# Kernel optimization log

Hardware: AMD Instinct MI355X
Metric: run time of the kernel (lower is better)

The kernel has to match this reference:

```python
import jax, jax.numpy as jnp
import numpy as np

N, E, IN, HID, OUT, H = 10000, 320000, 256, 128, 128, 4
SLOPE = 0.2

def setup_inputs() -> dict:
    key = jax.random.key(0)
    ks = jax.random.split(key, 12)
    s = lambda d: 1.0 / np.sqrt(d)
    return {
        "x": jax.random.normal(ks[0], (N, IN), jnp.float32),
        "edge_index": jax.random.randint(ks[1], (2, E), 0, N, jnp.int32),
        "W1": jax.random.normal(ks[2], (IN, H * HID), jnp.float32) * s(IN),
        "a_src1": jax.random.normal(ks[3], (H, HID), jnp.float32) * s(HID),
        "a_dst1": jax.random.normal(ks[4], (H, HID), jnp.float32) * s(HID),
        "b1": jnp.zeros((H * HID,), jnp.float32),
        "W2": jax.random.normal(ks[5], (H * HID, H * OUT), jnp.float32) * s(H * HID),
        "a_src2": jax.random.normal(ks[6], (H, OUT), jnp.float32) * s(OUT),
        "a_dst2": jax.random.normal(ks[7], (H, OUT), jnp.float32) * s(OUT),
        "b2": jnp.zeros((OUT,), jnp.float32),
    }

def _gat_layer(x, src, dst, W, a_src, a_dst, bias, concat, C):
    n = x.shape[0]
    h = (x @ W).reshape(n, H, C)                      # [N,H,C]
    alpha_s = jnp.einsum('nhc,hc->nh', h, a_src)      # [N,H]
    alpha_d = jnp.einsum('nhc,hc->nh', h, a_dst)
    e = jax.nn.leaky_relu(alpha_s[src] + alpha_d[dst], SLOPE)  # [E,H]
    # segment softmax over incoming edges of each dst node
    m = jax.ops.segment_max(e, dst, num_segments=n)   # [N,H]
    m = jnp.where(jnp.isfinite(m), m, 0.0)
    ex = jnp.exp(e - m[dst])
    denom = jax.ops.segment_sum(ex, dst, num_segments=n)
    alpha = ex / (denom[dst] + 1e-16)                 # [E,H]
    msg = h[src] * alpha[:, :, None]                  # [E,H,C]
    out = jax.ops.segment_sum(msg, dst, num_segments=n)  # [N,H,C]
    out = out.reshape(n, H * C) if concat else out.mean(axis=1)
    return out + bias

def reference(x, edge_index, W1, a_src1, a_dst1, b1, W2, a_src2, a_dst2, b2):
    n = x.shape[0]
    loops = jnp.arange(n, dtype=edge_index.dtype)
    src = jnp.concatenate([edge_index[0], loops])
    dst = jnp.concatenate([edge_index[1], loops])
    h = _gat_layer(x, src, dst, W1, a_src1, a_dst1, b1, True, HID)
    h = jax.nn.relu(h)  # dropout is identity in eval mode
    out = _gat_layer(h, src, dst, W2, a_src2, a_dst2, b2, False, OUT)
    return out
```

## Files before the change

kernel.cpp:

```cpp
#include <hip/hip_runtime.h>
#include <hip/hip_fp16.h>
#include <math.h>

#define Nn 10000
#define Ee 320000
#define EE 330000
#define INF_ 256
#define NH 4
#define OUTC 128
#define F1 512
#define F2 512
#define SLOPE 0.2f
#define STRIDE 80
#define LDK 40
#define NT 256
#define GRID 1024
#define GT (GRID * NT)
#define MT 157
#define GEMM_TILES (MT * NH)
#define PASS_VB ((Nn / 16) * NH)

static __device__ __forceinline__ float lrelu(float x) { return fmaxf(x, SLOPE * x); }

using frag_ab = __attribute__((ext_vector_type(8))) _Float16;
using frag_c  = __attribute__((ext_vector_type(4))) float;

struct Params {
    const float* x; const int* ei;
    const float* W1; const float* a_src1; const float* a_dst1; const float* b1;
    const float* W2; const float* a_src2; const float* a_dst2; const float* b2;
    float* out;
    int* counts; int* csr; int* bar;
    _Float16* hh; _Float16* aggh; _Float16* w1t; _Float16* w2t; _Float16* tmp;
    float* as1; float* ad1; float* as2; float* ad2;
};

static __device__ __forceinline__ void gbar(int* bar, int ph) {
    __syncthreads();
    if (threadIdx.x == 0) {
        __hip_atomic_fetch_add(&bar[ph], 1, __ATOMIC_ACQ_REL, __HIP_MEMORY_SCOPE_AGENT);
        while (__hip_atomic_load(&bar[ph], __ATOMIC_ACQUIRE, __HIP_MEMORY_SCOPE_AGENT) < GRID)
            __builtin_amdgcn_s_sleep(1);
    }
    __syncthreads();
}

static __device__ void prep0(const Params& p) {
    int gt = blockIdx.x * NT + threadIdx.x;
    for (int i = gt; i < Nn; i += GT) p.counts[i] = 0;
    for (int i = gt; i < F1 * INF_; i += GT) {
        int n = i >> 8, k = i & 255;
        p.w1t[i] = (_Float16)p.W1[(size_t)k * F1 + n];
    }
    for (int i = gt; i < F2 * F1; i += GT) {
        int n = i >> 9, k = i & 511;
        p.w2t[i] = (_Float16)p.W2[(size_t)k * F2 + n];
    }
}

static __device__ void scatter_edges(const Params& p, int bi, int nb) {
    for (int e = bi * NT + threadIdx.x; e < EE; e += nb * NT) {
        int src, dst;
        if (e < Ee) { src = p.ei[e]; dst = p.ei[Ee + e]; }
        else        { src = e - Ee; dst = e - Ee; }
        int slot = atomicAdd(&p.counts[dst], 1);
        if (slot < STRIDE) p.csr[dst * STRIDE + slot] = src;
    }
}

template <bool AF32>
static __device__ void gemm_tile(const _Float16* __restrict__ Ah,
                                 const float* __restrict__ Af,
                                 const _Float16* __restrict__ BT,
                                 _Float16* __restrict__ C,
                                 const float* __restrict__ a_src,
                                 const float* __restrict__ a_dst,
                                 float* __restrict__ as_out,
                                 float* __restrict__ ad_out,
                                 int K, int bmi, int head,
                                 _Float16* As, _Float16* Bs) {
    const int tid = threadIdx.x;
    const int wave = tid >> 6, lane = tid & 63;
    const int q = lane >> 4, ml = lane & 15;
    const int bm = bmi * 64, bn = head * 128;
    const int srow = tid >> 2, scol = (tid & 3) * 8;

    frag_c acc[8];
#pragma unroll
    for (int f = 0; f < 8; f++)
#pragma unroll
        for (int r = 0; r < 4; r++) acc[f][r] = 0.f;

    for (int k0 = 0; k0 < K; k0 += 32) {
        int gm = bm + srow;
        frag_ab av;
        if (gm < Nn) {
            if constexpr (AF32) {
                const float* Ap = Af + (size_t)gm * K + k0 + scol;
                float4 v0 = *(const float4*)Ap;
                float4 v1 = *(const float4*)(Ap + 4);
                av[0] = (_Float16)v0.x; av[1] = (_Float16)v0.y;
                av[2] = (_Float16)v0.z; av[3] = (_Float16)v0.w;
                av[4] = (_Float16)v1.x; av[5] = (_Float16)v1.y;
                av[6] = (_Float16)v1.z; av[7] = (_Float16)v1.w;
            } else {
                av = *(const frag_ab*)(Ah + (size_t)gm * K + k0 + scol);
            }
        } else {
#pragma unroll
            for (int j = 0; j < 8; j++) av[j] = (_Float16)0.f;
        }
        *(frag_ab*)&As[srow * LDK + scol] = av;
        *(frag_ab*)&Bs[srow * LDK + scol] =
            *(const frag_ab*)(BT + (size_t)(bn + srow) * K + k0 + scol);
        *(frag_ab*)&Bs[(64 + srow) * LDK + scol] =
            *(const frag_ab*)(BT + (size_t)(bn + 64 + srow) * K + k0 + scol);
        __syncthreads();
        frag_ab a = *(frag_ab*)&As[(wave * 16 + ml) * LDK + q * 8];
#pragma unroll
        for (int f = 0; f < 8; f++) {
            frag_ab b = *(frag_ab*)&Bs[(f * 16 + ml) * LDK + q * 8];
            acc[f] = __builtin_amdgcn_mfma_f32_16x16x32_f16(a, b, acc[f], 0, 0, 0);
        }
        __syncthreads();
    }
    float asum[4] = {}, dsum[4] = {};
#pragma unroll
    for (int f = 0; f < 8; f++) {
        int cl = f * 16 + ml;
        int col = bn + cl;
        float sa = a_src[head * 128 + cl];
        float da = a_dst[head * 128 + cl];
#pragma unroll
        for (int r = 0; r < 4; r++) {
            int row = bm + wave * 16 + q * 4 + r;
            if (row < Nn) C[(size_t)row * (NH * 128) + col] = (_Float16)acc[f][r];
            asum[r] += acc[f][r] * sa;
            dsum[r] += acc[f][r] * da;
        }
    }
#pragma unroll
    for (int r = 0; r < 4; r++) {
#pragma unroll
        for (int off = 1; off < 16; off <<= 1) {
            asum[r] += __shfl_xor(asum[r], off);
            dsum[r] += __shfl_xor(dsum[r], off);
        }
    }
    if (ml == 0) {
#pragma unroll
        for (int r = 0; r < 4; r++) {
            int row = bm + wave * 16 + q * 4 + r;
            if (row < Nn) {
                as_out[(size_t)head * Nn + row] = asum[r];
                ad_out[(size_t)head * Nn + row] = dsum[r];
            }
        }
    }
}

template <int LAYER>
static __device__ void pass_body(int vb, const int* __restrict__ counts,
                                 const int* __restrict__ csr,
                                 const float* __restrict__ as,
                                 const float* __restrict__ ad,
                                 const _Float16* __restrict__ hh,
                                 const float* __restrict__ b1,
                                 _Float16* __restrict__ outp, int2 (*ew)[84]) {
    int head = vb & 3;
    int qw = threadIdx.x >> 4;
    int l = threadIdx.x & 15;
    int n = (vb >> 2) * 16 + qw;
    int deg = counts[n]; if (deg > STRIDE) deg = STRIDE;
    int pdeg = (deg + 7) & ~7;
    const float* ash = as + (size_t)head * Nn;
    float adh = ad[(size_t)head * Nn + n];
    int base = n * STRIDE;
    float m = -1e30f;
    for (int k = l; k < pdeg; k += 16) {
        int src = 0; float v = -1e30f;
        if (k < deg) {
            src = csr[base + k];
            v = lrelu(ash[src] + adh);
        }
        ew[qw][k] = make_int2(src, __float_as_int(v));
        m = fmaxf(m, v);
    }
    m = fmaxf(m, __shfl_xor(m, 1));
    m = fmaxf(m, __shfl_xor(m, 2));
    m = fmaxf(m, __shfl_xor(m, 4));
    m = fmaxf(m, __shfl_xor(m, 8));
    float s = 0.f;
    for (int k = l; k < pdeg; k += 16) {
        float e = __expf(__int_as_float(ew[qw][k].y) - m);
        ew[qw][k].y = __float_as_int(e);
        s += e;
    }
    s += __shfl_xor(s, 1);
    s += __shfl_xor(s, 2);
    s += __shfl_xor(s, 4);
    s += __shfl_xor(s, 8);
    float inv = 1.f / (s + 1e-16f);
    int c = head * 128 + (l << 3);
    float acc[8] = {};
    for (int kk = 0; kk < pdeg; kk += 8) {
        int2 pj[8];
#pragma unroll
        for (int j = 0; j < 8; j++) pj[j] = ew[qw][kk + j];
#pragma unroll
        for (int j = 0; j < 8; j++) {
            float w = __int_as_float(pj[j].y);
            frag_ab r = *(const frag_ab*)(hh + (size_t)pj[j].x * 512 + c);
#pragma unroll
            for (int u = 0; u < 8; u++) acc[u] = fmaf((float)r[u], w, acc[u]);
        }
    }
    _Float16 oh[8];
    if constexpr (LAYER == 1) {
#pragma unroll
        for (int j = 0; j < 8; j++)
            oh[j] = (_Float16)fmaxf(acc[j] * inv + b1[c + j], 0.f);
    } else {
        float qq = 0.25f * inv;
#pragma unroll
        for (int j = 0; j < 8; j++) oh[j] = (_Float16)(acc[j] * qq);
    }
    *(float4*)&outp[(size_t)n * 512 + c] = *(float4*)oh;
}

static __device__ void reduce_out(const Params& p) {
    int gt = blockIdx.x * NT + threadIdx.x;
    for (int i = gt; i < Nn * OUTC; i += GT) {
        int n = i >> 7, oc = i & 127;
        const _Float16* tp = p.tmp + (size_t)n * 512 + oc;
        p.out[i] = (float)tp[0] + (float)tp[128] + (float)tp[256] + (float)tp[384] + p.b2[oc];
    }
}

__global__ __launch_bounds__(NT, 4) void mega(Params p) {
    __shared__ _Float16 As[64 * LDK];
    __shared__ _Float16 Bs[128 * LDK];
    __shared__ int2 ew[16][84];

    prep0(p);
    gbar(p.bar, 0);

    if (blockIdx.x < GEMM_TILES)
        gemm_tile<true>(nullptr, p.x, p.w1t, p.hh, p.a_src1, p.a_dst1, p.as1, p.ad1,
                        INF_, blockIdx.x % MT, blockIdx.x / MT, As, Bs);
    else
        scatter_edges(p, blockIdx.x - GEMM_TILES, GRID - GEMM_TILES);
    gbar(p.bar, 1);

    for (int vb = blockIdx.x; vb < PASS_VB; vb += GRID)
        pass_body<1>(vb, p.counts, p.csr, p.as1, p.ad1, p.hh, p.b1, p.aggh, ew);
    gbar(p.bar, 2);

    if (blockIdx.x < GEMM_TILES)
        gemm_tile<false>(p.aggh, nullptr, p.w2t, p.hh, p.a_src2, p.a_dst2, p.as2, p.ad2,
                         F1, blockIdx.x % MT, blockIdx.x / MT, As, Bs);
    gbar(p.bar, 3);

    for (int vb = blockIdx.x; vb < PASS_VB; vb += GRID)
        pass_body<2>(vb, p.counts, p.csr, p.as2, p.ad2, p.hh, nullptr, p.tmp, ew);
    gbar(p.bar, 4);

    reduce_out(p);
}

__global__ __launch_bounds__(NT) void k_p0(Params p) { prep0(p); }
__global__ __launch_bounds__(NT) void k_p1(Params p) {
    __shared__ _Float16 As[64 * LDK];
    __shared__ _Float16 Bs[128 * LDK];
    if (blockIdx.x < GEMM_TILES)
        gemm_tile<true>(nullptr, p.x, p.w1t, p.hh, p.a_src1, p.a_dst1, p.as1, p.ad1,
                        INF_, blockIdx.x % MT, blockIdx.x / MT, As, Bs);
    else
        scatter_edges(p, blockIdx.x - GEMM_TILES, GRID - GEMM_TILES);
}
__global__ __launch_bounds__(NT) void k_p2(Params p) {
    __shared__ int2 ew[16][84];
    for (int vb = blockIdx.x; vb < PASS_VB; vb += GRID)
        pass_body<1>(vb, p.counts, p.csr, p.as1, p.ad1, p.hh, p.b1, p.aggh, ew);
}
__global__ __launch_bounds__(NT) void k_p3(Params p) {
    __shared__ _Float16 As[64 * LDK];
    __shared__ _Float16 Bs[128 * LDK];
    if (blockIdx.x < GEMM_TILES)
        gemm_tile<false>(p.aggh, nullptr, p.w2t, p.hh, p.a_src2, p.a_dst2, p.as2, p.ad2,
                         F1, blockIdx.x % MT, blockIdx.x / MT, As, Bs);
}
__global__ __launch_bounds__(NT) void k_p4(Params p) {
    __shared__ int2 ew[16][84];
    for (int vb = blockIdx.x; vb < PASS_VB; vb += GRID)
        pass_body<2>(vb, p.counts, p.csr, p.as2, p.ad2, p.hh, nullptr, p.tmp, ew);
}
__global__ __launch_bounds__(NT) void k_p5(Params p) { reduce_out(p); }

extern "C" void kernel_launch(void* const* d_in, const int* in_sizes, int n_in,
                              void* d_out, int out_size, void* d_ws, size_t ws_size,
                              hipStream_t stream) {
    Params p;
    p.x      = (const float*)d_in[0];
    p.ei     = (const int*)d_in[1];
    p.W1     = (const float*)d_in[2];
    p.a_src1 = (const float*)d_in[3];
    p.a_dst1 = (const float*)d_in[4];
    p.b1     = (const float*)d_in[5];
    p.W2     = (const float*)d_in[6];
    p.a_src2 = (const float*)d_in[7];
    p.a_dst2 = (const float*)d_in[8];
    p.b2     = (const float*)d_in[9];
    p.out    = (float*)d_out;

    char* w = (char*)d_ws;
    p.tmp  = (_Float16*)w; w += (size_t)Nn * F2 * 2;
    p.hh   = (_Float16*)w; w += (size_t)Nn * F1 * 2;
    p.aggh = (_Float16*)w; w += (size_t)Nn * F1 * 2;
    p.w1t  = (_Float16*)w; w += (size_t)F1 * INF_ * 2;
    p.w2t  = (_Float16*)w; w += (size_t)F2 * F1 * 2;
    p.as1  = (float*)w;    w += (size_t)NH * Nn * 4;
    p.ad1  = (float*)w;    w += (size_t)NH * Nn * 4;
    p.as2  = (float*)w;    w += (size_t)NH * Nn * 4;
    p.ad2  = (float*)w;    w += (size_t)NH * Nn * 4;
    p.csr  = (int*)w;      w += (size_t)Nn * STRIDE * 4;
    p.counts = (int*)w;    w += (size_t)Nn * 4;
    p.bar  = (int*)w;      w += 8 * 4;

    static int occ = -1;
    if (occ < 0) {
        int nb = 0;
        if (hipOccupancyMaxActiveBlocksPerMultiprocessor(&nb, mega, NT, 0) != hipSuccess)
            nb = 0;
        occ = nb;
    }

    if (occ >= 4) {
        (void)hipMemsetAsync(p.bar, 0, 8 * sizeof(int), stream);
        mega<<<GRID, NT, 0, stream>>>(p);
    } else {
        k_p0<<<GRID, NT, 0, stream>>>(p);
        k_p1<<<GRID, NT, 0, stream>>>(p);
        k_p2<<<GRID, NT, 0, stream>>>(p);
        k_p3<<<GEMM_TILES, NT, 0, stream>>>(p);
        k_p4<<<GRID, NT, 0, stream>>>(p);
        k_p5<<<GRID, NT, 0, stream>>>(p);
    }
}
```

Baseline: 198.0 us.

## Size persistent grid from occupancy and alias shared memory between phases

The persistent megakernel now takes its grid size from the occupancy query (occ*256, capped at 1024) instead of a fixed 1024 blocks. The grid barrier reads gridDim, and the GEMM and edge-scatter work loops over tiles so any grid size covers the work. GEMM tiles and the edge-weight buffer now share one aliased shared-memory array, and the launch_bounds minimum-blocks hint is dropped, which may change register allocation and occupancy. The GEMM K-loop moves its trailing barrier to the top of the iteration. This makes the megakernel path usable when fewer than four blocks fit per CU, at the cost of fewer blocks doing more work each when occupancy is lower.

```diff
diff --git a/kernel.cpp b/kernel.cpp
--- a/kernel.cpp
+++ b/kernel.cpp
@@ -14,11 +14,11 @@
 #define STRIDE 80
 #define LDK 40
 #define NT 256
-#define GRID 1024
-#define GT (GRID * NT)
+#define GRID_MAX 1024
 #define MT 157
 #define GEMM_TILES (MT * NH)
 #define PASS_VB ((Nn / 16) * NH)
+#define SMEM_BYTES (192 * LDK * 2)
 
 static __device__ __forceinline__ float lrelu(float x) { return fmaxf(x, SLOPE * x); }
 
@@ -39,20 +39,21 @@
     __syncthreads();
     if (threadIdx.x == 0) {
         __hip_atomic_fetch_add(&bar[ph], 1, __ATOMIC_ACQ_REL, __HIP_MEMORY_SCOPE_AGENT);
-        while (__hip_atomic_load(&bar[ph], __ATOMIC_ACQUIRE, __HIP_MEMORY_SCOPE_AGENT) < GRID)
+        while (__hip_atomic_load(&bar[ph], __ATOMIC_ACQUIRE, __HIP_MEMORY_SCOPE_AGENT) <
+               (int)gridDim.x)
             __builtin_amdgcn_s_sleep(1);
     }
     __syncthreads();
 }
 
-static __device__ void prep0(const Params& p) {
+static __device__ void prep0(const Params& p, int gstride) {
     int gt = blockIdx.x * NT + threadIdx.x;
-    for (int i = gt; i < Nn; i += GT) p.counts[i] = 0;
-    for (int i = gt; i < F1 * INF_; i += GT) {
+    for (int i = gt; i < Nn; i += gstride) p.counts[i] = 0;
+    for (int i = gt; i < F1 * INF_; i += gstride) {
         int n = i >> 8, k = i & 255;
         p.w1t[i] = (_Float16)p.W1[(size_t)k * F1 + n];
     }
-    for (int i = gt; i < F2 * F1; i += GT) {
+    for (int i = gt; i < F2 * F1; i += gstride) {
         int n = i >> 9, k = i & 511;
         p.w2t[i] = (_Float16)p.W2[(size_t)k * F2 + n];
     }
@@ -110,6 +111,7 @@
 #pragma unroll
             for (int j = 0; j < 8; j++) av[j] = (_Float16)0.f;
         }
+        __syncthreads();
         *(frag_ab*)&As[srow * LDK + scol] = av;
         *(frag_ab*)&Bs[srow * LDK + scol] =
             *(const frag_ab*)(BT + (size_t)(bn + srow) * K + k0 + scol);
@@ -122,8 +124,8 @@
             frag_ab b = *(frag_ab*)&Bs[(f * 16 + ml) * LDK + q * 8];
             acc[f] = __builtin_amdgcn_mfma_f32_16x16x32_f16(a, b, acc[f], 0, 0, 0);
         }
-        __syncthreads();
-    }
+    }
+    __syncthreads();
     float asum[4] = {}, dsum[4] = {};
 #pragma unroll
     for (int f = 0; f < 8; f++) {
@@ -228,74 +230,85 @@
     *(float4*)&outp[(size_t)n * 512 + c] = *(float4*)oh;
 }
 
-static __device__ void reduce_out(const Params& p) {
+static __device__ void reduce_out(const Params& p, int gstride) {
     int gt = blockIdx.x * NT + threadIdx.x;
-    for (int i = gt; i < Nn * OUTC; i += GT) {
+    for (int i = gt; i < Nn * OUTC; i += gstride) {
         int n = i >> 7, oc = i & 127;
         const _Float16* tp = p.tmp + (size_t)n * 512 + oc;
         p.out[i] = (float)tp[0] + (float)tp[128] + (float)tp[256] + (float)tp[384] + p.b2[oc];
     }
 }
 
-__global__ __launch_bounds__(NT, 4) void mega(Params p) {
-    __shared__ _Float16 As[64 * LDK];
-    __shared__ _Float16 Bs[128 * LDK];
-    __shared__ int2 ew[16][84];
-
-    prep0(p);
+__global__ __launch_bounds__(NT) void mega(Params p) {
+    __shared__ __align__(16) char smem[SMEM_BYTES];
+    _Float16* As = (_Float16*)smem;
+    _Float16* Bs = (_Float16*)(smem + 64 * LDK * 2);
+    int2 (*ew)[84] = (int2(*)[84])smem;
+    const int grid = gridDim.x;
+    const int gstride = grid * NT;
+
+    prep0(p, gstride);
     gbar(p.bar, 0);
 
+    {
+        int nscat = (grid > GEMM_TILES) ? (grid - GEMM_TILES) : (grid >> 2);
+        int ngemm = grid - nscat;
+        if ((int)blockIdx.x < ngemm) {
+            for (int t = blockIdx.x; t < GEMM_TILES; t += ngemm)
+                gemm_tile<true>(nullptr, p.x, p.w1t, p.hh, p.a_src1, p.a_dst1,
+                                p.as1, p.ad1, INF_, t % MT, t / MT, As, Bs);
+        } else {
+            scatter_edges(p, blockIdx.x - ngemm, nscat);
+        }
+    }
+    gbar(p.bar, 1);
+
+    for (int vb = blockIdx.x; vb < PASS_VB; vb += grid)
+        pass_body<1>(vb, p.counts, p.csr, p.as1, p.ad1, p.hh, p.b1, p.aggh, ew);
+    gbar(p.bar, 2);
+
+    for (int t = blockIdx.x; t < GEMM_TILES; t += grid)
+        gemm_tile<false>(p.aggh, nullptr, p.w2t, p.hh, p.a_src2, p.a_dst2,
+                         p.as2, p.ad2, F1, t % MT, t / MT, As, Bs);
+    gbar(p.bar, 3);
+
+    for (int vb = blockIdx.x; vb < PASS_VB; vb += grid)
+        pass_body<2>(vb, p.counts, p.csr, p.as2, p.ad2, p.hh, nullptr, p.tmp, ew);
+    gbar(p.bar, 4);
+
+    reduce_out(p, gstride);
+}
+
+__global__ __launch_bounds__(NT) void k_p0(Params p) { prep0(p, GRID_MAX * NT); }
+__global__ __launch_bounds__(NT) void k_p1(Params p) {
+    __shared__ __align__(16) char smem[SMEM_BYTES];
+    _Float16* As = (_Float16*)smem;
+    _Float16* Bs = (_Float16*)(smem + 64 * LDK * 2);
     if (blockIdx.x < GEMM_TILES)
         gemm_tile<true>(nullptr, p.x, p.w1t, p.hh, p.a_src1, p.a_dst1, p.as1, p.ad1,
                         INF_, blockIdx.x % MT, blockIdx.x / MT, As, Bs);
     else
-        scatter_edges(p, blockIdx.x - GEMM_TILES, GRID - GEMM_TILES);
-    gbar(p.bar, 1);
-
-    for (int vb = blockIdx.x; vb < PASS_VB; vb += GRID)
+        scatter_edges(p, blockIdx.x - GEMM_TILES, GRID_MAX - GEMM_TILES);
+}
+__global__ __launch_bounds__(NT) void k_p2(Params p) {
+    __shared__ int2 ew[16][84];
+    for (int vb = blockIdx.x; vb < PASS_VB; vb += GRID_MAX)
         pass_body<1>(vb, p.counts, p.csr, p.as1, p.ad1, p.hh, p.b1, p.aggh, ew);
-    gbar(p.bar, 2);
-
+}
+__global__ __launch_bounds__(NT) void k_p3(Params p) {
+    __shared__ __align__(16) char smem[SMEM_BYTES];
+    _Float16* As = (_Float16*)smem;
+    _Float16* Bs = (_Float16*)(smem + 64 * LDK * 2);
     if (blockIdx.x < GEMM_TILES)
         gemm_tile<false>(p.aggh, nullptr, p.w2t, p.hh, p.a_src2, p.a_dst2, p.as2, p.ad2,
                          F1, blockIdx.x % MT, blockIdx.x / MT, As, Bs);
-    gbar(p.bar, 3);
-
-    for (int vb = blockIdx.x; vb < PASS_VB; vb += GRID)
-        pass_body<2>(vb, p.counts, p.csr, p.as2, p.ad2, p.hh, nullptr, p.tmp, ew);
-    gbar(p.bar, 4);
-
-    reduce_out(p);
-}
-
-__global__ __launch_bounds__(NT) void k_p0(Params p) { prep0(p); }
-__global__ __launch_bounds__(NT) void k_p1(Params p) {
-    __shared__ _Float16 As[64 * LDK];
-    __shared__ _Float16 Bs[128 * LDK];
-    if (blockIdx.x < GEMM_TILES)
-        gemm_tile<true>(nullptr, p.x, p.w1t, p.hh, p.a_src1, p.a_dst1, p.as1, p.ad1,
-                        INF_, blockIdx.x % MT, blockIdx.x / MT, As, Bs);
-    else
-        scatter_edges(p, blockIdx.x - GEMM_TILES, GRID - GEMM_TILES);
-}
-__global__ __launch_bounds__(NT) void k_p2(Params p) {
-    __shared__ int2 ew[16][84];
-    for (int vb = blockIdx.x; vb < PASS_VB; vb += GRID)
-        pass_body<1>(vb, p.counts, p.csr, p.as1, p.ad1, p.hh, p.b1, p.aggh, ew);
-}
-__global__ __launch_bounds__(NT) void k_p3(Params p) {
-    __shared__ _Float16 As[64 * LDK];
-    __shared__ _Float16 Bs[128 * LDK];
-    if (blockIdx.x < GEMM_TILES)
-        gemm_tile<false>(p.aggh, nullptr, p.w2t, p.hh, p.a_src2, p.a_dst2, p.as2, p.ad2,
-                         F1, blockIdx.x % MT, blockIdx.x / MT, As, Bs);
 }
 __global__ __launch_bounds__(NT) void k_p4(Params p) {
     __shared__ int2 ew[16][84];
-    for (int vb = blockIdx.x; vb < PASS_VB; vb += GRID)
+    for (int vb = blockIdx.x; vb < PASS_VB; vb += GRID_MAX)
         pass_body<2>(vb, p.counts, p.csr, p.as2, p.ad2, p.hh, nullptr, p.tmp, ew);
 }
-__global__ __launch_bounds__(NT) void k_p5(Params p) { reduce_out(p); }
+__global__ __launch_bounds__(NT) void k_p5(Params p) { reduce_out(p, GRID_MAX * NT); }
 
 extern "C" void kernel_launch(void* const* d_in, const int* in_sizes, int n_in,
                               void* d_out, int out_size, void* d_ws, size_t ws_size,
@@ -334,16 +347,18 @@
             nb = 0;
         occ = nb;
     }
-
-    if (occ >= 4) {
+    int grid = occ * 256;
+    if (grid > GRID_MAX) grid = GRID_MAX;
+
+    if (grid >= 256) {
         (void)hipMemsetAsync(p.bar, 0, 8 * sizeof(int), stream);
-        mega<<<GRID, NT, 0, stream>>>(p);
+        mega<<<grid, NT, 0, stream>>>(p);
     } else {
-        k_p0<<<GRID, NT, 0, stream>>>(p);
-        k_p1<<<GRID, NT, 0, stream>>>(p);
-        k_p2<<<GRID, NT, 0, stream>>>(p);
+        k_p0<<<GRID_MAX, NT, 0, stream>>>(p);
+        k_p1<<<GRID_MAX, NT, 0, stream>>>(p);
+        k_p2<<<GRID_MAX, NT, 0, stream>>>(p);
         k_p3<<<GEMM_TILES, NT, 0, stream>>>(p);
-        k_p4<<<GRID, NT, 0, stream>>>(p);
-        k_p5<<<GRID, NT, 0, stream>>>(p);
-    }
-}
+        k_p4<<<GRID_MAX, NT, 0, stream>>>(p);
+        k_p5<<<GRID_MAX, NT, 0, stream>>>(p);
+    }
+}
```

New measurement: 418.4 us. 2.11x slower.
